# Kernel tuning notes

Measured on AMD Instinct MI355X. Metric: run time of the kernel, lower is better.

The kernel has to match this reference:

```python
import jax, jax.numpy as jnp
import numpy as np

T = 2048
STATE_DIM = 1024
EMBED_DIM = 1024
HIDDEN = 150
MAX_WIDTH = 10


def setup_inputs() -> dict:
    key = jax.random.key(0)
    ks = jax.random.split(key, 6)
    scale = 0.02
    return {
        "embeds": jax.random.normal(ks[0], (T, EMBED_DIM), jnp.float32),
        "states": jax.random.normal(ks[1], (T, STATE_DIM), jnp.float32),
        "w1": jax.random.normal(ks[2], (HIDDEN, STATE_DIM), jnp.float32) * scale,
        "b1": jnp.zeros((HIDDEN,), jnp.float32),
        "w2": jax.random.normal(ks[3], (HIDDEN, HIDDEN), jnp.float32) * scale,
        "b2": jnp.zeros((HIDDEN,), jnp.float32),
        "w3": jax.random.normal(ks[4], (1, HIDDEN), jnp.float32) * scale,
        "b3": jnp.zeros((1,), jnp.float32),
    }


def reference(embeds, states, w1, b1, w2, b2, w3, b3):
    # SpanAttention MLP: per-token scalar score.
    h = jax.nn.relu(states @ w1.T + b1)
    h = jax.nn.relu(h @ w2.T + b2)
    attns = (h @ w3.T + b3)[:, 0]  # (T,)

    n_tok = states.shape[0]
    outs = []
    # Fixed set of span widths 1..10 (structural, not data-dependent).
    for n in range(1, MAX_WIDTH + 1):
        n_spans = n_tok - n + 1
        # (n_spans, n) window indices
        idx = jnp.arange(n_spans)[:, None] + jnp.arange(n)[None, :]
        # per-span softmax over the window
        a = jax.nn.softmax(attns[idx], axis=1)  # (n_spans, n)
        # attention-weighted sum of embeds over each window
        pooled = jnp.einsum("wn,wne->we", a, embeds[idx])  # (n_spans, E)
        # g = [start state, end state, pooled embed]
        g = jnp.concatenate([states[:n_spans], states[n - 1:], pooled], axis=-1)
        outs.append(g)
    # (sum_n (T-n+1), 2*STATE_DIM + EMBED_DIM)
    return jnp.concatenate(outs, axis=0)
```

## Files before the change

kernel.cpp:

```cpp
#include <hip/hip_runtime.h>

#define T 2048
#define SD 1024
#define ED 1024
#define HID 150
#define MAXW 10

typedef float f32x4 __attribute__((ext_vector_type(4)));

__global__ __launch_bounds__(256) void mlp_scores_kernel(
    const float* __restrict__ states,
    const float* __restrict__ w1, const float* __restrict__ b1,
    const float* __restrict__ w2, const float* __restrict__ b2,
    const float* __restrict__ w3, const float* __restrict__ b3,
    float* __restrict__ expA)
{
    const int t0 = blockIdx.x * 4;
    __shared__ float4 s_state[4][256];
    __shared__ float s_h1[4][192];
    __shared__ float s_h2[4][192];
    const int tid = threadIdx.x;

    for (int i = tid; i < 4 * 192; i += 256) {
        (&s_h1[0][0])[i] = 0.f;
        (&s_h2[0][0])[i] = 0.f;
    }
    {
        const float4* src = (const float4*)(states + (size_t)t0 * SD);
        float4* dst = &s_state[0][0];
        for (int i = tid; i < 4 * SD / 4; i += 256) dst[i] = src[i];
    }
    __syncthreads();

    const int lane = tid & 63;
    const int wave = tid >> 6;

    {
        int j = wave * 2;
        float4 wra[4], wrb[4];
        {
            const float4* w4a = (const float4*)(w1 + (size_t)j * SD);
#pragma unroll
            for (int m = 0; m < 4; ++m) {
                wra[m] = w4a[m * 64 + lane];
                wrb[m] = w4a[256 + m * 64 + lane];
            }
        }
        while (j < HID) {
            const int jn = j + 8;
            const int jp = (jn < HID) ? jn : j;
            float4 nra[4], nrb[4];
            {
                const float4* n4a = (const float4*)(w1 + (size_t)jp * SD);
#pragma unroll
                for (int m = 0; m < 4; ++m) {
                    nra[m] = n4a[m * 64 + lane];
                    nrb[m] = n4a[256 + m * 64 + lane];
                }
            }
            const float bja = b1[j];
            const float bjb = b1[j + 1];
#pragma unroll
            for (int t = 0; t < 4; ++t) {
                float acc0 = 0.f, acc1 = 0.f;
#pragma unroll
                for (int m = 0; m < 4; ++m) {
                    const float4 sv = s_state[t][m * 64 + lane];
                    acc0 += sv.x * wra[m].x + sv.y * wra[m].y
                          + sv.z * wra[m].z + sv.w * wra[m].w;
                    acc1 += sv.x * wrb[m].x + sv.y * wrb[m].y
                          + sv.z * wrb[m].z + sv.w * wrb[m].w;
                }
#pragma unroll
                for (int off = 32; off > 0; off >>= 1) {
                    acc0 += __shfl_down(acc0, off, 64);
                    acc1 += __shfl_down(acc1, off, 64);
                }
                if (lane == 0) {
                    s_h1[t][j]     = fmaxf(acc0 + bja, 0.f);
                    s_h1[t][j + 1] = fmaxf(acc1 + bjb, 0.f);
                }
            }
#pragma unroll
            for (int m = 0; m < 4; ++m) { wra[m] = nra[m]; wrb[m] = nrb[m]; }
            j = jn;
        }
    }
    __syncthreads();

    for (int j = wave; j < HID; j += 4) {
        const float* wrow = w2 + (size_t)j * HID;
        const float wa = wrow[lane];
        const float wb = wrow[lane + 64];
        const float wc = (lane + 128 < HID) ? wrow[lane + 128] : 0.f;
        const float bj = b2[j];
#pragma unroll
        for (int t = 0; t < 4; ++t) {
            float acc = s_h1[t][lane] * wa + s_h1[t][lane + 64] * wb
                      + s_h1[t][lane + 128] * wc;
#pragma unroll
            for (int off = 32; off > 0; off >>= 1) acc += __shfl_down(acc, off, 64);
            if (lane == 0) s_h2[t][j] = fmaxf(acc + bj, 0.f);
        }
    }
    __syncthreads();

    {
        const int t = wave;
        const float wa = w3[lane];
        const float wb = w3[lane + 64];
        const float wc = (lane + 128 < HID) ? w3[lane + 128] : 0.f;
        float acc = s_h2[t][lane] * wa + s_h2[t][lane + 64] * wb
                  + s_h2[t][lane + 128] * wc;
#pragma unroll
        for (int off = 32; off > 0; off >>= 1) acc += __shfl_down(acc, off, 64);
        if (lane == 0) expA[t0 + t] = expf(acc + b3[0]);
    }
}

__global__ __launch_bounds__(256) void span_kernel(
    const float* __restrict__ embeds,
    const float* __restrict__ states,
    const float* __restrict__ expA,
    float* __restrict__ out)
{
    const int s = blockIdx.x;
    const int c = threadIdx.x;

    const f32x4 st_s = ((const f32x4*)(states + (size_t)s * SD))[c];

    f32x4 P = (f32x4)(0.f);
    float S = 0.f;

    if (s <= T - MAXW) {
        int base = 0;
#pragma unroll
        for (int i = 0; i < MAXW; ++i) {
            const float E = expA[s + i];
            const f32x4 e  = ((const f32x4*)(embeds + (size_t)(s + i) * ED))[c];
            const f32x4 se = ((const f32x4*)(states + (size_t)(s + i) * SD))[c];
            P += E * e;
            S += E;
            const float inv = 1.f / S;
            f32x4* orow = (f32x4*)(out + (size_t)(base + s) * 3072);
            orow[c]       = st_s;
            orow[256 + c] = se;
            orow[512 + c] = P * inv;
            base += T - i;
        }
    } else {
        int base = 0;
        for (int i = 0; i < MAXW; ++i) {
            if (s + i < T) {
                const float E = expA[s + i];
                const f32x4 e  = ((const f32x4*)(embeds + (size_t)(s + i) * ED))[c];
                const f32x4 se = ((const f32x4*)(states + (size_t)(s + i) * SD))[c];
                P += E * e;
                S += E;
                const float inv = 1.f / S;
                f32x4* orow = (f32x4*)(out + (size_t)(base + s) * 3072);
                orow[c]       = st_s;
                orow[256 + c] = se;
                orow[512 + c] = P * inv;
            }
            base += T - i;
        }
    }
}

extern "C" void kernel_launch(void* const* d_in, const int* in_sizes, int n_in,
                              void* d_out, int out_size, void* d_ws, size_t ws_size,
                              hipStream_t stream) {
    const float* embeds = (const float*)d_in[0];
    const float* states = (const float*)d_in[1];
    const float* w1 = (const float*)d_in[2];
    const float* b1 = (const float*)d_in[3];
    const float* w2 = (const float*)d_in[4];
    const float* b2 = (const float*)d_in[5];
    const float* w3 = (const float*)d_in[6];
    const float* b3 = (const float*)d_in[7];
    float* out = (float*)d_out;
    float* expA = (float*)d_ws;

    mlp_scores_kernel<<<T / 4, 256, 0, stream>>>(states, w1, b1, w2, b2, w3, b3, expA);
    span_kernel<<<T, 256, 0, stream>>>(embeds, states, expA, out);
}
```

Before: 358.1 us.

## Reorganize span kernel by width with sliding windows and widen MLP blocks

```diff
diff --git a/kernel.cpp b/kernel.cpp
--- a/kernel.cpp
+++ b/kernel.cpp
@@ -8,7 +8,7 @@
 
 typedef float f32x4 __attribute__((ext_vector_type(4)));
 
-__global__ __launch_bounds__(256) void mlp_scores_kernel(
+__global__ __launch_bounds__(512) void mlp_scores_kernel(
     const float* __restrict__ states,
     const float* __restrict__ w1, const float* __restrict__ b1,
     const float* __restrict__ w2, const float* __restrict__ b2,
@@ -21,14 +21,14 @@
     __shared__ float s_h2[4][192];
     const int tid = threadIdx.x;
 
-    for (int i = tid; i < 4 * 192; i += 256) {
+    for (int i = tid; i < 4 * 192; i += 512) {
         (&s_h1[0][0])[i] = 0.f;
         (&s_h2[0][0])[i] = 0.f;
     }
     {
         const float4* src = (const float4*)(states + (size_t)t0 * SD);
         float4* dst = &s_state[0][0];
-        for (int i = tid; i < 4 * SD / 4; i += 256) dst[i] = src[i];
+        for (int i = tid; i < 4 * SD / 4; i += 512) dst[i] = src[i];
     }
     __syncthreads();
 
@@ -47,7 +47,7 @@
             }
         }
         while (j < HID) {
-            const int jn = j + 8;
+            const int jn = j + 16;
             const int jp = (jn < HID) ? jn : j;
             float4 nra[4], nrb[4];
             {
@@ -88,7 +88,7 @@
     }
     __syncthreads();
 
-    for (int j = wave; j < HID; j += 4) {
+    for (int j = wave; j < HID; j += 8) {
         const float* wrow = w2 + (size_t)j * HID;
         const float wa = wrow[lane];
         const float wb = wrow[lane + 64];
@@ -105,7 +105,7 @@
     }
     __syncthreads();
 
-    {
+    if (wave < 4) {
         const int t = wave;
         const float wa = w3[lane];
         const float wb = w3[lane + 64];
@@ -124,46 +124,48 @@
     const float* __restrict__ expA,
     float* __restrict__ out)
 {
-    const int s = blockIdx.x;
+    const int NB = 5112;
+    int b = blockIdx.x;
+    b = (b & 7) * (NB / 8) + (b >> 3);
+
+    const int bstart[11] = {0, 512, 1024, 1536, 2048, 2559, 3070, 3581, 4092, 4602, 5112};
+    const int rowoff[10] = {0, 2048, 4095, 6141, 8186, 10230, 12273, 14315, 16356, 18396};
+
+    int n = 1;
+#pragma unroll
+    for (int m = 2; m <= MAXW; ++m) if (b >= bstart[m - 1]) n = m;
+    const int s0 = (b - bstart[n - 1]) * 4;
+
     const int c = threadIdx.x;
-
-    const f32x4 st_s = ((const f32x4*)(states + (size_t)s * SD))[c];
+    const f32x4* emb4 = (const f32x4*)embeds;
+    const f32x4* st4  = (const f32x4*)states;
 
     f32x4 P = (f32x4)(0.f);
     float S = 0.f;
+    for (int i = 0; i < n; ++i) {
+        const float E = expA[s0 + i];
+        P += E * emb4[(size_t)(s0 + i) * 256 + c];
+        S += E;
+    }
 
-    if (s <= T - MAXW) {
-        int base = 0;
+    const int rowbase = rowoff[n - 1];
 #pragma unroll
-        for (int i = 0; i < MAXW; ++i) {
-            const float E = expA[s + i];
-            const f32x4 e  = ((const f32x4*)(embeds + (size_t)(s + i) * ED))[c];
-            const f32x4 se = ((const f32x4*)(states + (size_t)(s + i) * SD))[c];
-            P += E * e;
-            S += E;
-            const float inv = 1.f / S;
-            f32x4* orow = (f32x4*)(out + (size_t)(base + s) * 3072);
-            orow[c]       = st_s;
-            orow[256 + c] = se;
-            orow[512 + c] = P * inv;
-            base += T - i;
-        }
-    } else {
-        int base = 0;
-        for (int i = 0; i < MAXW; ++i) {
-            if (s + i < T) {
-                const float E = expA[s + i];
-                const f32x4 e  = ((const f32x4*)(embeds + (size_t)(s + i) * ED))[c];
-                const f32x4 se = ((const f32x4*)(states + (size_t)(s + i) * SD))[c];
-                P += E * e;
-                S += E;
-                const float inv = 1.f / S;
-                f32x4* orow = (f32x4*)(out + (size_t)(base + s) * 3072);
-                orow[c]       = st_s;
-                orow[256 + c] = se;
-                orow[512 + c] = P * inv;
-            }
-            base += T - i;
+    for (int g = 0; g < 4; ++g) {
+        const int s = s0 + g;
+        if (s > T - n) break;
+        const f32x4 stv = st4[(size_t)s * 256 + c];
+        const f32x4 sev = st4[(size_t)(s + n - 1) * 256 + c];
+        const float inv = __builtin_amdgcn_rcpf(S);
+        f32x4* orow = (f32x4*)(out + (size_t)(rowbase + s) * 3072);
+        orow[c]       = stv;
+        orow[256 + c] = sev;
+        orow[512 + c] = P * inv;
+        if (g < 3 && s + 1 <= T - n) {
+            const float Eo = expA[s];
+            const float Ei = expA[s + n];
+            P += Ei * emb4[(size_t)(s + n) * 256 + c]
+               - Eo * emb4[(size_t)s * 256 + c];
+            S += Ei - Eo;
         }
     }
 }
@@ -182,6 +184,6 @@
     float* out = (float*)d_out;
     float* expA = (float*)d_ws;
 
-    mlp_scores_kernel<<<T / 4, 256, 0, stream>>>(states, w1, b1, w2, b2, w3, b3, expA);
-    span_kernel<<<T, 256, 0, stream>>>(embeds, states, expA, out);
+    mlp_scores_kernel<<<T / 4, 512, 0, stream>>>(states, w1, b1, w2, b2, w3, b3, expA);
+    span_kernel<<<5112, 256, 0, stream>>>(embeds, states, expA, out);
 }
```

Result: slower. 382.6 us (+6.9%).
